# Kernel tuning notes

Measured on AMD Instinct MI355X. Metric: run time of the kernel, lower is better.

## Reference

```python
import jax, jax.numpy as jnp
import numpy as np

N = 1024      # params.input_dim (f1 is a square [N, N] similarity matrix)
TOPK = 16     # params.topk
B = 64        # hardcoded batch in the original reshape
W = 2 * N // B  # spatial width after reshape


def setup_inputs() -> dict:
    key = jax.random.key(0)
    k1, k2, k3 = jax.random.split(key, 3)
    f1 = jax.random.normal(k1, (N, N), dtype=jnp.float32)
    # Conv2d(in=N, out=N, kernel=(TOPK, 1)) weights, kaiming-ish scale
    conv_w = jax.random.normal(k2, (N, N, TOPK, 1), dtype=jnp.float32) * 0.01
    conv_b = jax.random.normal(k3, (N,), dtype=jnp.float32) * 0.01
    return {"f1": f1, "conv_w": conv_w, "conv_b": conv_b}


def reference(f1, conv_w, conv_b):
    # i = topk indices along last dim (largest, sorted) -> [N, TOPK]
    _, idx = jax.lax.top_k(f1, TOPK)
    # pos = f1[i]: gather rows of f1 by the topk column indices -> [N, TOPK, N]
    pos = f1[idx]
    # repeat_interleave(TOPK, dim=0).reshape(N, TOPK, -1) == each row tiled TOPK times
    rep = jnp.broadcast_to(f1[:, None, :], (N, TOPK, N))
    # cat on dim=2 -> [N, TOPK, 2N]; reshape to NCHW [B, N, TOPK, W]
    out = jnp.concatenate([rep, pos], axis=2).reshape(B, N, TOPK, W)
    # Conv2d kernel (TOPK, 1), VALID padding collapses H -> 1: [B, N, 1, W]
    y = jax.lax.conv_general_dilated(
        out, conv_w, window_strides=(1, 1), padding='VALID',
        dimension_numbers=('NCHW', 'OIHW', 'NCHW'))
    y = y + conv_b[None, :, None, None]
    return jax.nn.relu(y).reshape(N, -1)  # [N, B*W] = [N, 2N]
```

## Files before the change

kernel.cpp:

```cpp
#include <hip/hip_runtime.h>
#include <stdint.h>


#define NDIM 1024
#define TK   16
#define KPOS 8192
#define KREP 512
#define NCOL 2048

typedef unsigned short u16;
typedef uint32_t u32;
typedef u16   u16x8  __attribute__((ext_vector_type(8)));
typedef __bf16 bf16x8 __attribute__((ext_vector_type(8)));
typedef float  f32x4  __attribute__((ext_vector_type(4)));

__device__ __forceinline__ u16 f2bf(float x) {
    union { float f; unsigned u; } v; v.f = x;
    unsigned r = 0x7FFFu + ((v.u >> 16) & 1u);
    return (u16)((v.u + r) >> 16);
}

__device__ __forceinline__ void load_lds_16B(const u16* g, u16* l) {
    __builtin_amdgcn_global_load_lds(
        (__attribute__((address_space(1))) void*)(uintptr_t)g,
        (__attribute__((address_space(3))) void*)(unsigned)(uintptr_t)l,
        16, 0, 0);
}

#define PREP_TOPK 256
#define PREP_ZERO 512
#define PREP_W    1024
#define PREP_F1T  256

__global__ __launch_bounds__(256) void prep_kernel(const float* __restrict__ f1,
                                                   const float* __restrict__ W,
                                                   int* __restrict__ idx,
                                                   u16* __restrict__ Wb,
                                                   u16* __restrict__ W1b,
                                                   u16* __restrict__ f1t,
                                                   float* __restrict__ out) {
    const int bid = blockIdx.x;
    const int t = threadIdx.x;
    if (bid < PREP_TOPK) {
        const int lane = t & 63;
        const int row  = bid * 4 + (t >> 6);
        float v[16];
        const float* src = f1 + row * NDIM + lane;
        #pragma unroll
        for (int j = 0; j < 16; ++j) v[j] = src[j * 64];
        for (int sel = 0; sel < TK; ++sel) {
            float best = -3.402823466e38f; int bg = 0x7fffffff;
            #pragma unroll
            for (int j = 0; j < 16; ++j)
                if (v[j] > best) { best = v[j]; bg = j * 64 + lane; }
            #pragma unroll
            for (int s = 1; s < 64; s <<= 1) {
                float ov = __shfl_xor(best, s);
                int   og = __shfl_xor(bg, s);
                if (ov > best || (ov == best && og < bg)) { best = ov; bg = og; }
            }
            if (lane == sel) idx[row * TK + sel] = bg;
            #pragma unroll
            for (int j = 0; j < 16; ++j)
                if (bg == j * 64 + lane) v[j] = -3.402823466e38f;
        }
    } else if (bid < PREP_TOPK + PREP_ZERO) {
        const int zb = bid - PREP_TOPK;
        f32x4 z = {0.f, 0.f, 0.f, 0.f};
        float* p = out + (size_t)zb * 4096 + t * 16;
        #pragma unroll
        for (int j = 0; j < 4; ++j) *(f32x4*)(p + j * 4) = z;
    } else if (bid < PREP_TOPK + PREP_ZERO + PREP_W) {
        const int o = bid - PREP_TOPK - PREP_ZERO;
        const float* wrow = W + (size_t)o * 16384;
        u16* wbrow = Wb + (size_t)o * KPOS;
        #pragma unroll
        for (int j = 0; j < 4; ++j) {
            const int v = j * 2048 + t * 8;
            const int u = ((v >> 5) << 6) + 32 + (v & 31);
            float4 a = *(const float4*)(wrow + u);
            float4 b = *(const float4*)(wrow + u + 4);
            u16x8 ov;
            ov[0] = f2bf(a.x); ov[1] = f2bf(a.y); ov[2] = f2bf(a.z); ov[3] = f2bf(a.w);
            ov[4] = f2bf(b.x); ov[5] = f2bf(b.y); ov[6] = f2bf(b.z); ov[7] = f2bf(b.w);
            *(u16x8*)(wbrow + v) = ov;
        }
        #pragma unroll
        for (int h = 0; h < 2; ++h) {
            const int kr = h * 256 + t;
            const int nl = kr >> 5, e = kr & 31;
            const float* base = wrow + nl * 1024 + e;
            float s = 0.f;
            #pragma unroll
            for (int tt = 0; tt < 16; ++tt) s += base[tt * 64];
            W1b[o * KREP + kr] = f2bf(s);
        }
    } else {
        const int gb = bid - PREP_TOPK - PREP_ZERO - PREP_W;
        const int unit = t >> 5;
        const int w = t & 31;
        const int rq = gb * 8 + unit;
        const int row = rq >> 1, q = rq & 1;
        const float* src = f1 + row * NDIM + q * 512;
        const int swp = ((w >> 2) & 1) * 8;
        u16 tmp[16];
        #pragma unroll
        for (int kh = 0; kh < 16; ++kh)
            tmp[kh ^ swp] = f2bf(src[kh * 32 + w]);
        u16* dst = f1t + ((size_t)row * 2 + q) * 512 + w * 16;
        *(u16x8*)(dst)     = *(u16x8*)(tmp);
        *(u16x8*)(dst + 8) = *(u16x8*)(tmp + 8);
    }
}

#define BM 128
#define BN 128
#define BK 64
#define KITERS 17

__global__ __launch_bounds__(256, 4) void gemm_kernel(const u16* __restrict__ Ap,
                                                      const u16* __restrict__ A1,
                                                      const u16* __restrict__ f1t,
                                                      const int* __restrict__ idx,
                                                      float* __restrict__ out) {
    __shared__ __align__(16) u16 As[2][BM * BK];
    __shared__ __align__(8) int idxO[272];
    const int f = blockIdx.x;
    const int m = f & 7;
    const int g = f >> 3;
    const int n = g & 15;
    const int z = g >> 4;
    const int t    = threadIdx.x;
    const int lane = t & 63;
    const int wave = t >> 6;
    const int wm   = (wave >> 1) * 64;
    const int wn   = (wave & 1) * 64;
    const int quad = lane >> 4;
    const int l16  = lane & 15;
    const int sw   = l16 & 7;
    const int o0 = m * BM;
    const int n0 = n * BN;
    const int nb0 = n * 4;
    const int kb = z * 1024;

    {
        const int j = t >> 2, bl = t & 3;
        const int ip = z * 64 + j;
        const int nl = ip >> 5, tt = (ip >> 1) & 15, q = ip & 1;
        const int row = idx[((nb0 + bl) * 16 + nl) * TK + tt];
        idxO[j * 4 + bl] = ((row << 1) + q) << 9;
        if (t < 16) {
            const int ci = t >> 2, bl2 = t & 3;
            const int ur = z * 4 + ci;
            const int rrow = (nb0 + bl2) * 16 + (ur >> 1);
            idxO[(64 + ci) * 4 + bl2] = ((rrow << 1) + (ur & 1)) << 9;
        }
    }

    f32x4 acc[4][4] = {};

    const int rA = t >> 3;
    const int c8 = t & 7;
    const int csw = (c8 ^ (rA & 7)) * 8;
    const u16* gApos = Ap + (size_t)(o0 + rA) * KPOS + kb + csw;
    const u16* gArep = A1 + (size_t)(o0 + rA) * KREP + z * 64 + csw;

    auto stage = [&](int it, int nb) {
        u16* lA = As[nb] + t * 8;
        if (it < 16) {
            const int k0 = it * BK;
            #pragma unroll
            for (int c = 0; c < 4; ++c)
                load_lds_16B(gApos + (size_t)(c * 32) * KPOS + k0, lA + c * 2048);
        } else {
            #pragma unroll
            for (int c = 0; c < 4; ++c)
                load_lds_16B(gArep + (size_t)(c * 32) * KREP, lA + c * 2048);
        }
    };

    const int qh = quad & 1;
    const int sel = (qh ^ ((l16 >> 2) & 1)) * 8;
    const u16* Bb0 = f1t + l16 * 16 + sel;
    const u16* Bb1 = f1t + (16 + l16) * 16 + sel;
    const int ci2base = quad >> 1;
    const int blh = (wave & 1) * 2;

    stage(0, 0);
    __syncthreads();

    for (int it = 0; it < KITERS; ++it) {
        const int cur = it & 1;
        if (it + 1 < KITERS) stage(it + 1, 1 - cur);

        const int jb = (it < 16) ? it * 4 : 64;
        #pragma unroll
        for (int ks = 0; ks < 2; ++ks) {
            const int2 offp = *(const int2*)(&idxO[(jb + ks * 2 + ci2base) * 4 + blh]);
            bf16x8 af[4], bfr[4];
            #pragma unroll
            for (int mt = 0; mt < 4; ++mt) {
                u16x8 bits = *(const u16x8*)(As[cur] + (wm + mt * 16 + l16) * BK
                                                + (((ks * 4 + quad) ^ sw) * 8));
                af[mt] = __builtin_bit_cast(bf16x8, bits);
            }
            #pragma unroll
            for (int nt = 0; nt < 4; ++nt) {
                const int off = (nt & 2) ? offp.y : offp.x;
                const u16* p = ((nt & 1) ? Bb1 : Bb0) + off;
                bfr[nt] = __builtin_bit_cast(bf16x8, *(const u16x8*)p);
            }
            #pragma unroll
            for (int mt = 0; mt < 4; ++mt)
                #pragma unroll
                for (int nt = 0; nt < 4; ++nt)
                    acc[mt][nt] = __builtin_amdgcn_mfma_f32_16x16x32_bf16(
                        af[mt], bfr[nt], acc[mt][nt], 0, 0, 0);
        }
        __syncthreads();
    }

    #pragma unroll
    for (int nt = 0; nt < 4; ++nt) {
        const int nn = n0 + wn + nt * 16 + l16;
        const int bb = nn >> 5, w = nn & 31;
        #pragma unroll
        for (int mt = 0; mt < 4; ++mt) {
            #pragma unroll
            for (int r = 0; r < 4; ++r) {
                const int o = o0 + wm + mt * 16 + quad * 4 + r;
                unsafeAtomicAdd(out + (size_t)(bb * 16 + (o >> 6)) * 2048
                                    + (o & 63) * 32 + w,
                                acc[mt][nt][r]);
            }
        }
    }
}

__global__ __launch_bounds__(256) void finalize_kernel(float* __restrict__ out,
                                                       const float* __restrict__ bias) {
    const int tid = blockIdx.x * 256 + threadIdx.x;
    const int f = tid * 4;
    const int o = ((f >> 11) & 15) * 64 + ((f & 2047) >> 5);
    const float bv = bias[o];
    float4 x = *(float4*)(out + f);
    x.x = fmaxf(x.x + bv, 0.f);
    x.y = fmaxf(x.y + bv, 0.f);
    x.z = fmaxf(x.z + bv, 0.f);
    x.w = fmaxf(x.w + bv, 0.f);
    *(float4*)(out + f) = x;
}

extern "C" void kernel_launch(void* const* d_in, const int* in_sizes, int n_in,
                              void* d_out, int out_size, void* d_ws, size_t ws_size,
                              hipStream_t stream) {
    const float* f1   = (const float*)d_in[0];
    const float* Wc   = (const float*)d_in[1];
    const float* bias = (const float*)d_in[2];
    float* out = (float*)d_out;

    int* idx = (int*)d_ws;
    u16* Wb  = (u16*)((char*)d_ws + 65536);
    u16* W1b = (u16*)((char*)d_ws + 16842752);
    u16* f1t = (u16*)((char*)d_ws + 17891328);

    prep_kernel<<<PREP_TOPK + PREP_ZERO + PREP_W + PREP_F1T,
                  256, 0, stream>>>(f1, Wc, idx, Wb, W1b, f1t, out);
    gemm_kernel<<<1024, 256, 0, stream>>>(Wb, W1b, f1t, idx, out);
    finalize_kernel<<<(NDIM * NCOL) / (4 * 256), 256, 0, stream>>>(out, bias);
}
```

Baseline: 184.0 us.

## Stage gathered B tiles in LDS and single-buffer A tiles

The gathered B operand (rows of the transposed f1 picked by the top-k indices) is now copied into double-buffered LDS with global_load_lds each iteration, instead of every lane reading it from global memory. The A tile becomes single-buffered, is loaded at the start of each iteration, and is followed by a barrier before compute. This replaces scattered per-lane global reads of B with shared LDS reads, but it exposes A load latency because A is no longer prefetched. The larger LDS footprint also means launch bounds drop from 4 to 3 blocks per CU.

```diff
diff --git a/kernel.cpp b/kernel.cpp
--- a/kernel.cpp
+++ b/kernel.cpp
@@ -118,12 +118,13 @@
 #define BK 64
 #define KITERS 17
 
-__global__ __launch_bounds__(256, 4) void gemm_kernel(const u16* __restrict__ Ap,
+__global__ __launch_bounds__(256, 3) void gemm_kernel(const u16* __restrict__ Ap,
                                                       const u16* __restrict__ A1,
                                                       const u16* __restrict__ f1t,
                                                       const int* __restrict__ idx,
                                                       float* __restrict__ out) {
-    __shared__ __align__(16) u16 As[2][BM * BK];
+    __shared__ __align__(16) u16 As[BM * BK];
+    __shared__ __align__(16) u16 Bs[2][16 * 512];
     __shared__ __align__(8) int idxO[272];
     const int f = blockIdx.x;
     const int m = f & 7;
@@ -141,7 +142,6 @@
     const int o0 = m * BM;
     const int n0 = n * BN;
     const int nb0 = n * 4;
-    const int kb = z * 1024;
 
     {
         const int j = t >> 2, bl = t & 3;
@@ -162,11 +162,11 @@
     const int rA = t >> 3;
     const int c8 = t & 7;
     const int csw = (c8 ^ (rA & 7)) * 8;
-    const u16* gApos = Ap + (size_t)(o0 + rA) * KPOS + kb + csw;
+    const u16* gApos = Ap + (size_t)(o0 + rA) * KPOS + z * 1024 + csw;
     const u16* gArep = A1 + (size_t)(o0 + rA) * KREP + z * 64 + csw;
 
-    auto stage = [&](int it, int nb) {
-        u16* lA = As[nb] + t * 8;
+    auto stageA = [&](int it) {
+        u16* lA = As + t * 8;
         if (it < 16) {
             const int k0 = it * BK;
             #pragma unroll
@@ -179,36 +179,41 @@
         }
     };
 
-    const int qh = quad & 1;
-    const int sel = (qh ^ ((l16 >> 2) & 1)) * 8;
-    const u16* Bb0 = f1t + l16 * 16 + sel;
-    const u16* Bb1 = f1t + (16 + l16) * 16 + sel;
-    const int ci2base = quad >> 1;
-    const int blh = (wave & 1) * 2;
-
-    stage(0, 0);
+    auto stageB = [&](int it, int nb) {
+        const int u0 = (it < 16) ? (it * 4 + wave) : (64 + wave);
+        #pragma unroll
+        for (int bl = 0; bl < 4; ++bl)
+            load_lds_16B(f1t + idxO[u0 * 4 + bl] + lane * 8,
+                         Bs[nb] + (wave * 4 + bl) * 512);
+    };
+
     __syncthreads();
+    stageB(0, 0);
 
     for (int it = 0; it < KITERS; ++it) {
         const int cur = it & 1;
-        if (it + 1 < KITERS) stage(it + 1, 1 - cur);
-
-        const int jb = (it < 16) ? it * 4 : 64;
+        stageA(it);
+        if (it + 1 < KITERS) stageB(it + 1, 1 - cur);
+        __syncthreads();
+
         #pragma unroll
         for (int ks = 0; ks < 2; ++ks) {
-            const int2 offp = *(const int2*)(&idxO[(jb + ks * 2 + ci2base) * 4 + blh]);
             bf16x8 af[4], bfr[4];
             #pragma unroll
             for (int mt = 0; mt < 4; ++mt) {
-                u16x8 bits = *(const u16x8*)(As[cur] + (wm + mt * 16 + l16) * BK
+                u16x8 bits = *(const u16x8*)(As + (wm + mt * 16 + l16) * BK
                                                 + (((ks * 4 + quad) ^ sw) * 8));
                 af[mt] = __builtin_bit_cast(bf16x8, bits);
             }
+            const int ci2 = ks * 2 + (quad >> 1);
+            const int qh  = quad & 1;
             #pragma unroll
             for (int nt = 0; nt < 4; ++nt) {
-                const int off = (nt & 2) ? offp.y : offp.x;
-                const u16* p = ((nt & 1) ? Bb1 : Bb0) + off;
-                bfr[nt] = __builtin_bit_cast(bf16x8, *(const u16x8*)p);
+                const int nn = wn + nt * 16 + l16;
+                const int blocf = nn >> 5, w = nn & 31;
+                u16x8 bits = *(const u16x8*)(Bs[cur] + (ci2 * 4 + blocf) * 512 + w * 16
+                                                + ((qh ^ ((w >> 2) & 1)) * 8));
+                bfr[nt] = __builtin_bit_cast(bf16x8, bits);
             }
             #pragma unroll
             for (int mt = 0; mt < 4; ++mt)
```

After: 184.2 us. About the same (+0.1%).

## Enlarge GEMM tiles to 256x256 with LDS-staged gathered B and interleaved pipeline

Applied to the files above, without the earlier changes.

The GEMM now uses 256x256 tiles with 512-thread blocks instead of 128x128 with 256 threads. The gathered B operand (f1t rows picked by top-k index) is staged into LDS through async global-to-LDS loads, where before each wave read it straight from global memory. The K loop is split into four phases that interleave staging with MFMA blocks, using explicit vmcnt waits, barriers and setprio, and the block-to-XCD mapping is changed. This aims to improve operand reuse and hide load latency, at the cost of more LDS, fewer resident blocks and a grid of only 256 blocks.

```diff
diff --git a/kernel.cpp b/kernel.cpp
--- a/kernel.cpp
+++ b/kernel.cpp
@@ -113,111 +113,161 @@
     }
 }
 
-#define BM 128
-#define BN 128
+#define BM 256
+#define BN 256
 #define BK 64
-#define KITERS 17
-
-__global__ __launch_bounds__(256, 4) void gemm_kernel(const u16* __restrict__ Ap,
+
+__global__ __launch_bounds__(512, 2) void gemm_kernel(const u16* __restrict__ Ap,
                                                       const u16* __restrict__ A1,
                                                       const u16* __restrict__ f1t,
                                                       const int* __restrict__ idx,
                                                       float* __restrict__ out) {
     __shared__ __align__(16) u16 As[2][BM * BK];
-    __shared__ __align__(8) int idxO[272];
+    __shared__ __align__(16) u16 Bs[2][32 * 512];
+    __shared__ __align__(8) int idxO[544];
+
     const int f = blockIdx.x;
-    const int m = f & 7;
-    const int g = f >> 3;
-    const int n = g & 15;
-    const int z = g >> 4;
+    const int xcd = f & 7;
+    const int m  = xcd >> 1;
+    const int zl = xcd & 1;
+    const int g  = f >> 3;
+    const int n  = g & 7;
+    const int zh = g >> 3;
+    const int z  = zh * 2 + zl;
     const int t    = threadIdx.x;
     const int lane = t & 63;
     const int wave = t >> 6;
-    const int wm   = (wave >> 1) * 64;
-    const int wn   = (wave & 1) * 64;
+    const int wm   = (wave >> 2) * 128;
+    const int wn   = (wave & 3) * 64;
     const int quad = lane >> 4;
     const int l16  = lane & 15;
     const int sw   = l16 & 7;
+    const int qh   = quad & 1;
     const int o0 = m * BM;
     const int n0 = n * BN;
-    const int nb0 = n * 4;
-    const int kb = z * 1024;
+    const int nb0 = n * 8;
 
     {
-        const int j = t >> 2, bl = t & 3;
-        const int ip = z * 64 + j;
+        const int uu = t >> 3, bl = t & 7;
+        const int ip = z * 64 + uu;
         const int nl = ip >> 5, tt = (ip >> 1) & 15, q = ip & 1;
         const int row = idx[((nb0 + bl) * 16 + nl) * TK + tt];
-        idxO[j * 4 + bl] = ((row << 1) + q) << 9;
-        if (t < 16) {
-            const int ci = t >> 2, bl2 = t & 3;
-            const int ur = z * 4 + ci;
+        idxO[t] = ((row << 1) + q) << 9;
+        if (t < 32) {
+            const int uur = t >> 3, bl2 = t & 7;
+            const int ur = z * 4 + uur;
             const int rrow = (nb0 + bl2) * 16 + (ur >> 1);
-            idxO[(64 + ci) * 4 + bl2] = ((rrow << 1) + (ur & 1)) << 9;
-        }
-    }
-
-    f32x4 acc[4][4] = {};
-
-    const int rA = t >> 3;
-    const int c8 = t & 7;
-    const int csw = (c8 ^ (rA & 7)) * 8;
-    const u16* gApos = Ap + (size_t)(o0 + rA) * KPOS + kb + csw;
-    const u16* gArep = A1 + (size_t)(o0 + rA) * KREP + z * 64 + csw;
-
-    auto stage = [&](int it, int nb) {
-        u16* lA = As[nb] + t * 8;
-        if (it < 16) {
-            const int k0 = it * BK;
-            #pragma unroll
-            for (int c = 0; c < 4; ++c)
-                load_lds_16B(gApos + (size_t)(c * 32) * KPOS + k0, lA + c * 2048);
+            idxO[512 + t] = ((rrow << 1) + (ur & 1)) << 9;
+        }
+    }
+
+    f32x4 acc[8][4] = {};
+
+    const int r0 = t >> 3;
+    const int c0 = t & 7;
+    const int csw = (c0 ^ (r0 & 7)) * 8;
+
+    auto stageA = [&](int tt1, int h, int nb) {
+        u16* dst = &As[nb][h * 8192 + wave * 512];
+        if (tt1 < 16) {
+            const u16* s0 = Ap + (size_t)(o0 + h * 128 + r0) * KPOS
+                               + z * 1024 + tt1 * 64 + csw;
+            load_lds_16B(s0, dst);
+            load_lds_16B(s0 + (size_t)64 * KPOS, dst + 4096);
         } else {
-            #pragma unroll
-            for (int c = 0; c < 4; ++c)
-                load_lds_16B(gArep + (size_t)(c * 32) * KREP, lA + c * 2048);
+            const u16* s0 = A1 + (size_t)(o0 + h * 128 + r0) * KREP
+                               + z * 64 + csw;
+            load_lds_16B(s0, dst);
+            load_lds_16B(s0 + (size_t)64 * KREP, dst + 4096);
         }
     };
 
-    const int qh = quad & 1;
-    const int sel = (qh ^ ((l16 >> 2) & 1)) * 8;
-    const u16* Bb0 = f1t + l16 * 16 + sel;
-    const u16* Bb1 = f1t + (16 + l16) * 16 + sel;
-    const int ci2base = quad >> 1;
-    const int blh = (wave & 1) * 2;
-
-    stage(0, 0);
+    auto stageB = [&](int tt1, int kk, int nb) {
+        #pragma unroll
+        for (int j = 0; j < 2; ++j) {
+            const int ci = kk * 2 + j;
+            const int uu = (tt1 < 16) ? (tt1 * 4 + ci) : (64 + ci);
+            const int off = idxO[uu * 8 + wave];
+            load_lds_16B(f1t + off + lane * 8,
+                         &Bs[nb][(ci * 8 + wave) * 512]);
+        }
+    };
+
+#define LOAD_A(MH, KS)                                                        \
+    {                                                                         \
+        _Pragma("unroll")                                                     \
+        for (int mt = 0; mt < 4; ++mt) {                                      \
+            const int row = wm + (MH) * 64 + mt * 16 + l16;                   \
+            u16x8 bits = *(const u16x8*)(Acur + row * 64                      \
+                                         + ((((KS) * 4 + quad) ^ sw) * 8));   \
+            af[mt] = __builtin_bit_cast(bf16x8, bits);                        \
+        }                                                                     \
+    }
+
+#define LOAD_B(KS)                                                            \
+    {                                                                         \
+        const int ci = (KS) * 2 + (quad >> 1);                                \
+        _Pragma("unroll")                                                     \
+        for (int nt = 0; nt < 4; ++nt) {                                      \
+            const int nn = wn + nt * 16 + l16;                                \
+            const int bl = nn >> 5, w = nn & 31;                              \
+            u16x8 bits = *(const u16x8*)(Bcur + (ci * 8 + bl) * 512 + w * 16  \
+                                         + ((qh ^ ((w >> 2) & 1)) * 8));      \
+            bfr[nt] = __builtin_bit_cast(bf16x8, bits);                       \
+        }                                                                     \
+    }
+
+#define MFMA_BLK(MH)                                                          \
+    {                                                                         \
+        __builtin_amdgcn_s_setprio(1);                                        \
+        _Pragma("unroll")                                                     \
+        for (int mt = 0; mt < 4; ++mt)                                        \
+            _Pragma("unroll")                                                 \
+            for (int nt = 0; nt < 4; ++nt)                                    \
+                acc[(MH) * 4 + mt][nt] = __builtin_amdgcn_mfma_f32_16x16x32_bf16( \
+                    af[mt], bfr[nt], acc[(MH) * 4 + mt][nt], 0, 0, 0);        \
+        __builtin_amdgcn_s_setprio(0);                                        \
+    }
+
     __syncthreads();
-
-    for (int it = 0; it < KITERS; ++it) {
-        const int cur = it & 1;
-        if (it + 1 < KITERS) stage(it + 1, 1 - cur);
-
-        const int jb = (it < 16) ? it * 4 : 64;
-        #pragma unroll
-        for (int ks = 0; ks < 2; ++ks) {
-            const int2 offp = *(const int2*)(&idxO[(jb + ks * 2 + ci2base) * 4 + blh]);
-            bf16x8 af[4], bfr[4];
-            #pragma unroll
-            for (int mt = 0; mt < 4; ++mt) {
-                u16x8 bits = *(const u16x8*)(As[cur] + (wm + mt * 16 + l16) * BK
-                                                + (((ks * 4 + quad) ^ sw) * 8));
-                af[mt] = __builtin_bit_cast(bf16x8, bits);
-            }
-            #pragma unroll
-            for (int nt = 0; nt < 4; ++nt) {
-                const int off = (nt & 2) ? offp.y : offp.x;
-                const u16* p = ((nt & 1) ? Bb1 : Bb0) + off;
-                bfr[nt] = __builtin_bit_cast(bf16x8, *(const u16x8*)p);
-            }
-            #pragma unroll
-            for (int mt = 0; mt < 4; ++mt)
-                #pragma unroll
-                for (int nt = 0; nt < 4; ++nt)
-                    acc[mt][nt] = __builtin_amdgcn_mfma_f32_16x16x32_bf16(
-                        af[mt], bfr[nt], acc[mt][nt], 0, 0, 0);
-        }
-        __syncthreads();
+    stageA(0, 0, 0); stageA(0, 1, 0);
+    stageB(0, 0, 0); stageB(0, 1, 0);
+    asm volatile("s_waitcnt vmcnt(0)" ::: "memory");
+    __builtin_amdgcn_s_barrier();
+
+    for (int tk = 0; tk < 17; ++tk) {
+        const int cur = tk & 1, nxt = cur ^ 1;
+        const int tn = tk + 1;
+        const u16* Acur = As[cur];
+        const u16* Bcur = Bs[cur];
+        bf16x8 af[4], bfr[4];
+
+        if (tn <= 16) stageA(tn, 0, nxt);
+        LOAD_B(0)
+        LOAD_A(0, 0)
+        MFMA_BLK(0)
+        __builtin_amdgcn_s_barrier();
+
+        if (tn <= 16) stageA(tn, 1, nxt);
+        if (tk < 16) { asm volatile("s_waitcnt vmcnt(4)" ::: "memory"); }
+        else         { asm volatile("s_waitcnt vmcnt(0)" ::: "memory"); }
+        LOAD_A(1, 0)
+        MFMA_BLK(1)
+        __builtin_amdgcn_s_barrier();
+
+        if (tn <= 16) stageB(tn, 0, nxt);
+        LOAD_B(1)
+        LOAD_A(0, 1)
+        MFMA_BLK(0)
+        __builtin_amdgcn_s_barrier();
+
+        if (tn <= 16) {
+            stageB(tn, 1, nxt);
+            asm volatile("s_waitcnt vmcnt(2)" ::: "memory");
+        }
+        LOAD_A(1, 1)
+        MFMA_BLK(1)
+        __builtin_amdgcn_s_barrier();
     }
 
     #pragma unroll
@@ -225,16 +275,19 @@
         const int nn = n0 + wn + nt * 16 + l16;
         const int bb = nn >> 5, w = nn & 31;
         #pragma unroll
-        for (int mt = 0; mt < 4; ++mt) {
+        for (int mi = 0; mi < 8; ++mi) {
             #pragma unroll
             for (int r = 0; r < 4; ++r) {
-                const int o = o0 + wm + mt * 16 + quad * 4 + r;
+                const int o = o0 + wm + mi * 16 + quad * 4 + r;
                 unsafeAtomicAdd(out + (size_t)(bb * 16 + (o >> 6)) * 2048
                                     + (o & 63) * 32 + w,
-                                acc[mt][nt][r]);
+                                acc[mi][nt][r]);
             }
         }
     }
+#undef LOAD_A
+#undef LOAD_B
+#undef MFMA_BLK
 }
 
 __global__ __launch_bounds__(256) void finalize_kernel(float* __restrict__ out,
@@ -266,6 +319,6 @@
 
     prep_kernel<<<PREP_TOPK + PREP_ZERO + PREP_W + PREP_F1T,
                   256, 0, stream>>>(f1, Wc, idx, Wb, W1b, f1t, out);
-    gemm_kernel<<<1024, 256, 0, stream>>>(Wb, W1b, f1t, idx, out);
+    gemm_kernel<<<256, 512, 0, stream>>>(Wb, W1b, f1t, idx, out);
     finalize_kernel<<<(NDIM * NCOL) / (4 * 256), 256, 0, stream>>>(out, bias);
 }
```

Result: slower. 188.2 us (+2.3%).
